# Performance work log

Hardware: AMD Instinct MI355X
Metric: run time of the kernel (lower is better)

## Reference

```python
import jax, jax.numpy as jnp
import numpy as np


def smooth_l1(x, y):
    d = jnp.abs(x - y)
    return jnp.where(d < 1.0, 0.5 * d * d, d - 0.5)


def setup_inputs() -> dict:
    key = jax.random.key(0)
    k1, k2, k3 = jax.random.split(key, 3)
    B, T, N, D = 4, 28, 1024, 3
    X_v = jax.random.normal(k1, (B, T, N, D), dtype=jnp.float32)
    target_X_v = jax.random.normal(k2, (B, T, N, D), dtype=jnp.float32)
    weights = jax.random.uniform(k3, (B, T), dtype=jnp.float32)
    return {"X_v": X_v, "target_X_v": target_X_v, "weights": weights}


def reference(X_v, target_X_v, weights):
    B = X_v.shape[0]
    # Pairwise squared distances [B,T,N,N] via ||p||^2 + ||t||^2 - 2 p.t
    pn = jnp.sum(X_v * X_v, axis=-1)                 # [B,T,N]
    tn = jnp.sum(target_X_v * target_X_v, axis=-1)   # [B,T,N]
    dist = (pn[..., :, None] + tn[..., None, :]
            - 2.0 * jnp.einsum('btnd,btmd->btnm', X_v, target_X_v))
    minv = jnp.argmin(dist, axis=-1)                 # [B,T,N] int
    # gather nearest target point for each pred point
    tagp = jnp.take_along_axis(target_X_v, minv[..., None], axis=2)  # [B,T,N,3]
    # per-(b,t) mean smooth-L1 over N points x 3 coords
    loss_bt = jnp.mean(smooth_l1(X_v, tagp), axis=(-2, -1))          # [B,T]
    loss = jnp.sum(loss_bt * weights) / B

    prec = jnp.mean(X_v, axis=2)        # [B,T,3]
    tarc = jnp.mean(target_X_v, axis=2) # [B,T,3]
    lossc = jnp.sum(smooth_l1(prec, tarc)) / (B * 3)
    return (loss, lossc)
```

## Files before the change

kernel.cpp:

```cpp
#include <hip/hip_runtime.h>

constexpr int Bc = 4;
constexpr int Tc = 28;
constexpr int Nc = 1024;
constexpr int Dc = 3;
constexpr int BT = Bc * Tc;
constexpr float OFFS = 512.0f;

constexpr int WS_PARTIAL = 0;
constexpr int WS_PSUM    = 224;
constexpr int WS_TSUM    = 224 + 224*3;

__device__ __forceinline__ float sl1(float d) {
    d = fabsf(d);
    return d < 1.0f ? 0.5f * d * d : d - 0.5f;
}

__global__ __launch_bounds__(256) void chamfer_kernel(
    const float* __restrict__ X, const float* __restrict__ Tg,
    const float* __restrict__ W, float* __restrict__ ws)
{
    __shared__ float4 sT4[Nc];
    __shared__ float sred[4][8];

    const int bt  = blockIdx.x >> 1;
    const int ph  = blockIdx.x & 1;
    const int tid = threadIdx.x;

    const float* xb = X + (size_t)bt * (Nc * Dc);
    const int n0 = ph * 512 + tid;
    const int n1 = n0 + 256;
    const float pAx = xb[n0 * 3 + 0], pAy = xb[n0 * 3 + 1], pAz = xb[n0 * 3 + 2];
    const float pBx = xb[n1 * 3 + 0], pBy = xb[n1 * 3 + 1], pBz = xb[n1 * 3 + 2];

    const float4* tg4 = (const float4*)(Tg + (size_t)bt * (Nc * Dc));
    const float4 r0 = tg4[3 * tid + 0];
    const float4 r1 = tg4[3 * tid + 1];
    const float4 r2 = tg4[3 * tid + 2];
    sT4[4 * tid + 0] = make_float4(r0.x, r0.y, r0.z, fmaf(r0.x, r0.x, fmaf(r0.y, r0.y, fmaf(r0.z, r0.z, OFFS))));
    sT4[4 * tid + 1] = make_float4(r0.w, r1.x, r1.y, fmaf(r0.w, r0.w, fmaf(r1.x, r1.x, fmaf(r1.y, r1.y, OFFS))));
    sT4[4 * tid + 2] = make_float4(r1.z, r1.w, r2.x, fmaf(r1.z, r1.z, fmaf(r1.w, r1.w, fmaf(r2.x, r2.x, OFFS))));
    sT4[4 * tid + 3] = make_float4(r2.y, r2.z, r2.w, fmaf(r2.y, r2.y, fmaf(r2.z, r2.z, fmaf(r2.w, r2.w, OFFS))));
    const float tsx = r0.x + r0.w + r1.z + r2.y;
    const float tsy = r0.y + r1.x + r1.w + r2.z;
    const float tsz = r0.z + r1.y + r2.x + r2.w;
    __syncthreads();

    const float cA0 = -2.0f * pAx, cA1 = -2.0f * pAy, cA2 = -2.0f * pAz;
    const float cB0 = -2.0f * pBx, cB1 = -2.0f * pBy, cB2 = -2.0f * pBz;

    float bestA = 3.4e38f, bestB = 3.4e38f;
    int iA = 0, iB = 0;

    constexpr int PF = 8;
    float4 bufA[PF], bufB[PF];

    #pragma unroll
    for (int j = 0; j < PF; ++j) bufA[j] = sT4[j];

    for (int m0 = 0; m0 < Nc; m0 += 2 * PF) {
        #pragma unroll
        for (int j = 0; j < PF; ++j) bufB[j] = sT4[m0 + PF + j];
        #pragma unroll
        for (int j = 0; j < PF; ++j) {
            const float4 t = bufA[j];
            const int m = m0 + j;
            float vA = fmaf(cA0, t.x, fmaf(cA1, t.y, fmaf(cA2, t.z, t.w)));
            float vB = fmaf(cB0, t.x, fmaf(cB1, t.y, fmaf(cB2, t.z, t.w)));
            bool ca = vA < bestA; bestA = ca ? vA : bestA; iA = ca ? m : iA;
            bool cb = vB < bestB; bestB = cb ? vB : bestB; iB = cb ? m : iB;
        }
        #pragma unroll
        for (int j = 0; j < PF; ++j) bufA[j] = sT4[(m0 + 2 * PF + j) & (Nc - 1)];
        #pragma unroll
        for (int j = 0; j < PF; ++j) {
            const float4 t = bufB[j];
            const int m = m0 + PF + j;
            float vA = fmaf(cA0, t.x, fmaf(cA1, t.y, fmaf(cA2, t.z, t.w)));
            float vB = fmaf(cB0, t.x, fmaf(cB1, t.y, fmaf(cB2, t.z, t.w)));
            bool ca = vA < bestA; bestA = ca ? vA : bestA; iA = ca ? m : iA;
            bool cb = vB < bestB; bestB = cb ? vB : bestB; iB = cb ? m : iB;
        }
    }

    const float4 tA = sT4[iA];
    const float4 tB = sT4[iB];
    float s = sl1(pAx - tA.x) + sl1(pAy - tA.y) + sl1(pAz - tA.z)
            + sl1(pBx - tB.x) + sl1(pBy - tB.y) + sl1(pBz - tB.z);

    float vals[7] = { s, pAx + pBx, pAy + pBy, pAz + pBz, tsx, tsy, tsz };
    const int lane = tid & 63, wid = tid >> 6;
    #pragma unroll
    for (int k = 0; k < 7; ++k) {
        float v = vals[k];
        #pragma unroll
        for (int off = 32; off; off >>= 1) v += __shfl_down(v, off, 64);
        if (lane == 0) sred[wid][k] = v;
    }
    __syncthreads();
    if (tid == 0) {
        float tot[7];
        #pragma unroll
        for (int k = 0; k < 7; ++k)
            tot[k] = sred[0][k] + sred[1][k] + sred[2][k] + sred[3][k];
        ws[WS_PARTIAL + blockIdx.x] = tot[0] * W[bt];
        ws[WS_PSUM + blockIdx.x * 3 + 0] = tot[1];
        ws[WS_PSUM + blockIdx.x * 3 + 1] = tot[2];
        ws[WS_PSUM + blockIdx.x * 3 + 2] = tot[3];
        if (ph == 0) {
            ws[WS_TSUM + bt * 3 + 0] = tot[4];
            ws[WS_TSUM + bt * 3 + 1] = tot[5];
            ws[WS_TSUM + bt * 3 + 2] = tot[6];
        }
    }
}

__global__ __launch_bounds__(256) void finalize_kernel(
    const float* __restrict__ ws, float* __restrict__ out)
{
    __shared__ float sred[4][2];
    const int tid = threadIdx.x;

    float lp = (tid < 224) ? ws[WS_PARTIAL + tid] : 0.0f;

    float lc = 0.0f;
    if (tid < BT) {
        const float inv = 1.0f / Nc;
        #pragma unroll
        for (int c = 0; c < 3; ++c) {
            float pm = (ws[WS_PSUM + (2 * tid) * 3 + c] + ws[WS_PSUM + (2 * tid + 1) * 3 + c]) * inv;
            float tm = ws[WS_TSUM + tid * 3 + c] * inv;
            lc += sl1(pm - tm);
        }
    }

    const int lane = tid & 63, wid = tid >> 6;
    #pragma unroll
    for (int off = 32; off; off >>= 1) {
        lp += __shfl_down(lp, off, 64);
        lc += __shfl_down(lc, off, 64);
    }
    if (lane == 0) { sred[wid][0] = lp; sred[wid][1] = lc; }
    __syncthreads();
    if (tid == 0) {
        float tlp = sred[0][0] + sred[1][0] + sred[2][0] + sred[3][0];
        float tlc = sred[0][1] + sred[1][1] + sred[2][1] + sred[3][1];
        out[0] = tlp * (1.0f / (Nc * Dc)) * (1.0f / Bc);
        out[1] = tlc * (1.0f / (Bc * Dc));
    }
}

extern "C" void kernel_launch(void* const* d_in, const int* in_sizes, int n_in,
                              void* d_out, int out_size, void* d_ws, size_t ws_size,
                              hipStream_t stream) {
    const float* X  = (const float*)d_in[0];
    const float* Tg = (const float*)d_in[1];
    const float* W  = (const float*)d_in[2];
    float* out = (float*)d_out;
    float* ws  = (float*)d_ws;

    chamfer_kernel<<<BT * 2, 256, 0, stream>>>(X, Tg, W, ws);
    finalize_kernel<<<1, 256, 0, stream>>>(ws, out);
}
```

Before: 88.61 us.

## Pack targets in a prep kernel and read them via uniform global loads

Adds a prep kernel that packs the target points with their squared norms into a float4 workspace and computes the centroid sums. The main kernel drops its shared-memory staging and barrier and reads the packed targets straight from global memory, where every lane loads the same address (a broadcast that should become scalar or cached loads). This aims to remove LDS traffic from the inner loop, but it adds one kernel launch and a workspace round trip. The OFFS bias added to the norms is also removed.

```diff
diff --git a/kernel.cpp b/kernel.cpp
--- a/kernel.cpp
+++ b/kernel.cpp
@@ -5,24 +5,71 @@
 constexpr int Nc = 1024;
 constexpr int Dc = 3;
 constexpr int BT = Bc * Tc;
-constexpr float OFFS = 512.0f;
 
-constexpr int WS_PARTIAL = 0;
-constexpr int WS_PSUM    = 224;
-constexpr int WS_TSUM    = 224 + 224*3;
+constexpr size_t WS_PACKED_F4 = 0;
+constexpr size_t WS_PARTIAL   = (size_t)BT * Nc * 4;
+constexpr size_t WS_PSUM      = WS_PARTIAL + 224;
+constexpr size_t WS_TSUM      = WS_PSUM + BT * 3;
 
 __device__ __forceinline__ float sl1(float d) {
     d = fabsf(d);
     return d < 1.0f ? 0.5f * d * d : d - 0.5f;
 }
 
+__global__ __launch_bounds__(256) void prep_kernel(
+    const float* __restrict__ X, const float* __restrict__ Tg,
+    float4* __restrict__ packed, float* __restrict__ sums)
+{
+    __shared__ float sred[4][8];
+    const int bt  = blockIdx.x;
+    const int tid = threadIdx.x;
+
+    const float4* tg4 = (const float4*)(Tg + (size_t)bt * (Nc * Dc));
+    const float4 r0 = tg4[3 * tid + 0];
+    const float4 r1 = tg4[3 * tid + 1];
+    const float4 r2 = tg4[3 * tid + 2];
+    float4* pk = packed + (size_t)bt * Nc;
+    pk[4 * tid + 0] = make_float4(r0.x, r0.y, r0.z, fmaf(r0.x, r0.x, fmaf(r0.y, r0.y, r0.z * r0.z)));
+    pk[4 * tid + 1] = make_float4(r0.w, r1.x, r1.y, fmaf(r0.w, r0.w, fmaf(r1.x, r1.x, r1.y * r1.y)));
+    pk[4 * tid + 2] = make_float4(r1.z, r1.w, r2.x, fmaf(r1.z, r1.z, fmaf(r1.w, r1.w, r2.x * r2.x)));
+    pk[4 * tid + 3] = make_float4(r2.y, r2.z, r2.w, fmaf(r2.y, r2.y, fmaf(r2.z, r2.z, r2.w * r2.w)));
+
+    const float4* x4 = (const float4*)(X + (size_t)bt * (Nc * Dc));
+    const float4 a0 = x4[3 * tid + 0];
+    const float4 a1 = x4[3 * tid + 1];
+    const float4 a2 = x4[3 * tid + 2];
+
+    float vals[6] = {
+        a0.x + a0.w + a1.z + a2.y,
+        a0.y + a1.x + a1.w + a2.z,
+        a0.z + a1.y + a2.x + a2.w,
+        r0.x + r0.w + r1.z + r2.y,
+        r0.y + r1.x + r1.w + r2.z,
+        r0.z + r1.y + r2.x + r2.w
+    };
+    const int lane = tid & 63, wid = tid >> 6;
+    #pragma unroll
+    for (int k = 0; k < 6; ++k) {
+        float v = vals[k];
+        #pragma unroll
+        for (int off = 32; off; off >>= 1) v += __shfl_down(v, off, 64);
+        if (lane == 0) sred[wid][k] = v;
+    }
+    __syncthreads();
+    if (tid == 0) {
+        #pragma unroll
+        for (int k = 0; k < 3; ++k) {
+            sums[WS_PSUM - WS_PARTIAL + bt * 3 + k] = sred[0][k] + sred[1][k] + sred[2][k] + sred[3][k];
+            sums[WS_TSUM - WS_PARTIAL + bt * 3 + k] = sred[0][k + 3] + sred[1][k + 3] + sred[2][k + 3] + sred[3][k + 3];
+        }
+    }
+}
+
 __global__ __launch_bounds__(256) void chamfer_kernel(
-    const float* __restrict__ X, const float* __restrict__ Tg,
-    const float* __restrict__ W, float* __restrict__ ws)
+    const float* __restrict__ X, const float4* __restrict__ packed,
+    const float* __restrict__ W, float* __restrict__ partial)
 {
-    __shared__ float4 sT4[Nc];
-    __shared__ float sred[4][8];
-
+    __shared__ float sred[4];
     const int bt  = blockIdx.x >> 1;
     const int ph  = blockIdx.x & 1;
     const int tid = threadIdx.x;
@@ -33,21 +80,10 @@
     const float pAx = xb[n0 * 3 + 0], pAy = xb[n0 * 3 + 1], pAz = xb[n0 * 3 + 2];
     const float pBx = xb[n1 * 3 + 0], pBy = xb[n1 * 3 + 1], pBz = xb[n1 * 3 + 2];
 
-    const float4* tg4 = (const float4*)(Tg + (size_t)bt * (Nc * Dc));
-    const float4 r0 = tg4[3 * tid + 0];
-    const float4 r1 = tg4[3 * tid + 1];
-    const float4 r2 = tg4[3 * tid + 2];
-    sT4[4 * tid + 0] = make_float4(r0.x, r0.y, r0.z, fmaf(r0.x, r0.x, fmaf(r0.y, r0.y, fmaf(r0.z, r0.z, OFFS))));
-    sT4[4 * tid + 1] = make_float4(r0.w, r1.x, r1.y, fmaf(r0.w, r0.w, fmaf(r1.x, r1.x, fmaf(r1.y, r1.y, OFFS))));
-    sT4[4 * tid + 2] = make_float4(r1.z, r1.w, r2.x, fmaf(r1.z, r1.z, fmaf(r1.w, r1.w, fmaf(r2.x, r2.x, OFFS))));
-    sT4[4 * tid + 3] = make_float4(r2.y, r2.z, r2.w, fmaf(r2.y, r2.y, fmaf(r2.z, r2.z, fmaf(r2.w, r2.w, OFFS))));
-    const float tsx = r0.x + r0.w + r1.z + r2.y;
-    const float tsy = r0.y + r1.x + r1.w + r2.z;
-    const float tsz = r0.z + r1.y + r2.x + r2.w;
-    __syncthreads();
-
     const float cA0 = -2.0f * pAx, cA1 = -2.0f * pAy, cA2 = -2.0f * pAz;
     const float cB0 = -2.0f * pBx, cB1 = -2.0f * pBy, cB2 = -2.0f * pBz;
+
+    const float4* __restrict__ pk = packed + (size_t)bt * Nc;
 
     float bestA = 3.4e38f, bestB = 3.4e38f;
     int iA = 0, iB = 0;
@@ -56,11 +92,11 @@
     float4 bufA[PF], bufB[PF];
 
     #pragma unroll
-    for (int j = 0; j < PF; ++j) bufA[j] = sT4[j];
+    for (int j = 0; j < PF; ++j) bufA[j] = pk[j];
 
     for (int m0 = 0; m0 < Nc; m0 += 2 * PF) {
         #pragma unroll
-        for (int j = 0; j < PF; ++j) bufB[j] = sT4[m0 + PF + j];
+        for (int j = 0; j < PF; ++j) bufB[j] = pk[m0 + PF + j];
         #pragma unroll
         for (int j = 0; j < PF; ++j) {
             const float4 t = bufA[j];
@@ -71,7 +107,7 @@
             bool cb = vB < bestB; bestB = cb ? vB : bestB; iB = cb ? m : iB;
         }
         #pragma unroll
-        for (int j = 0; j < PF; ++j) bufA[j] = sT4[(m0 + 2 * PF + j) & (Nc - 1)];
+        for (int j = 0; j < PF; ++j) bufA[j] = pk[(m0 + 2 * PF + j) & (Nc - 1)];
         #pragma unroll
         for (int j = 0; j < PF; ++j) {
             const float4 t = bufB[j];
@@ -83,53 +119,35 @@
         }
     }
 
-    const float4 tA = sT4[iA];
-    const float4 tB = sT4[iB];
+    const float4 tA = pk[iA];
+    const float4 tB = pk[iB];
     float s = sl1(pAx - tA.x) + sl1(pAy - tA.y) + sl1(pAz - tA.z)
             + sl1(pBx - tB.x) + sl1(pBy - tB.y) + sl1(pBz - tB.z);
 
-    float vals[7] = { s, pAx + pBx, pAy + pBy, pAz + pBz, tsx, tsy, tsz };
     const int lane = tid & 63, wid = tid >> 6;
     #pragma unroll
-    for (int k = 0; k < 7; ++k) {
-        float v = vals[k];
-        #pragma unroll
-        for (int off = 32; off; off >>= 1) v += __shfl_down(v, off, 64);
-        if (lane == 0) sred[wid][k] = v;
-    }
+    for (int off = 32; off; off >>= 1) s += __shfl_down(s, off, 64);
+    if (lane == 0) sred[wid] = s;
     __syncthreads();
-    if (tid == 0) {
-        float tot[7];
-        #pragma unroll
-        for (int k = 0; k < 7; ++k)
-            tot[k] = sred[0][k] + sred[1][k] + sred[2][k] + sred[3][k];
-        ws[WS_PARTIAL + blockIdx.x] = tot[0] * W[bt];
-        ws[WS_PSUM + blockIdx.x * 3 + 0] = tot[1];
-        ws[WS_PSUM + blockIdx.x * 3 + 1] = tot[2];
-        ws[WS_PSUM + blockIdx.x * 3 + 2] = tot[3];
-        if (ph == 0) {
-            ws[WS_TSUM + bt * 3 + 0] = tot[4];
-            ws[WS_TSUM + bt * 3 + 1] = tot[5];
-            ws[WS_TSUM + bt * 3 + 2] = tot[6];
-        }
-    }
+    if (tid == 0)
+        partial[blockIdx.x] = (sred[0] + sred[1] + sred[2] + sred[3]) * W[bt];
 }
 
 __global__ __launch_bounds__(256) void finalize_kernel(
-    const float* __restrict__ ws, float* __restrict__ out)
+    const float* __restrict__ sums, float* __restrict__ out)
 {
     __shared__ float sred[4][2];
     const int tid = threadIdx.x;
 
-    float lp = (tid < 224) ? ws[WS_PARTIAL + tid] : 0.0f;
+    float lp = (tid < 224) ? sums[tid] : 0.0f;
 
     float lc = 0.0f;
     if (tid < BT) {
         const float inv = 1.0f / Nc;
         #pragma unroll
         for (int c = 0; c < 3; ++c) {
-            float pm = (ws[WS_PSUM + (2 * tid) * 3 + c] + ws[WS_PSUM + (2 * tid + 1) * 3 + c]) * inv;
-            float tm = ws[WS_TSUM + tid * 3 + c] * inv;
+            float pm = sums[WS_PSUM - WS_PARTIAL + tid * 3 + c] * inv;
+            float tm = sums[WS_TSUM - WS_PARTIAL + tid * 3 + c] * inv;
             lc += sl1(pm - tm);
         }
     }
@@ -157,8 +175,11 @@
     const float* Tg = (const float*)d_in[1];
     const float* W  = (const float*)d_in[2];
     float* out = (float*)d_out;
-    float* ws  = (float*)d_ws;
 
-    chamfer_kernel<<<BT * 2, 256, 0, stream>>>(X, Tg, W, ws);
-    finalize_kernel<<<1, 256, 0, stream>>>(ws, out);
+    float4* packed = (float4*)d_ws;
+    float*  sums   = (float*)d_ws + WS_PARTIAL;
+
+    prep_kernel<<<BT, 256, 0, stream>>>(X, Tg, packed, sums);
+    chamfer_kernel<<<BT * 2, 256, 0, stream>>>(X, packed, W, sums );
+    finalize_kernel<<<1, 256, 0, stream>>>(sums, out);
 }
```

New measurement: 105.5 us. +19.1%, slower.

## Split target search into quarters across blocks with separate gather kernel

Applied to the files above, without the earlier changes.

The nearest-neighbour search is split so each block scans only a quarter of the target points, which raises the grid from 224 to 896 blocks to fill more compute units. Per-quarter best values and indices go to global workspace, and a new gather kernel picks the global argmin, gathers the target point and does the smooth-L1 reduction. This adds a kernel launch and global traffic for the partial results, and it drops the constant offset previously added to the squared norm. The __syncthreads sits inside a block-uniform branch (th==0), so it is safe.

```diff
diff --git a/kernel.cpp b/kernel.cpp
--- a/kernel.cpp
+++ b/kernel.cpp
@@ -5,26 +5,30 @@
 constexpr int Nc = 1024;
 constexpr int Dc = 3;
 constexpr int BT = Bc * Tc;
-constexpr float OFFS = 512.0f;
-
-constexpr int WS_PARTIAL = 0;
-constexpr int WS_PSUM    = 224;
-constexpr int WS_TSUM    = 224 + 224*3;
+constexpr int QT = 256;
+
+constexpr size_t WS_BESTV   = 0;
+constexpr size_t WS_BESTI   = (size_t)BT * Nc * 4;
+constexpr size_t WS_PARTIAL = WS_BESTI + (size_t)BT * Nc * 4;
+constexpr size_t WS_PSUM    = WS_PARTIAL + 224;
+constexpr size_t WS_TSUM    = WS_PSUM + BT * 2 * 3;
 
 __device__ __forceinline__ float sl1(float d) {
     d = fabsf(d);
     return d < 1.0f ? 0.5f * d * d : d - 0.5f;
 }
 
-__global__ __launch_bounds__(256) void chamfer_kernel(
+__global__ __launch_bounds__(256) void chamfer_quarter_kernel(
     const float* __restrict__ X, const float* __restrict__ Tg,
-    const float* __restrict__ W, float* __restrict__ ws)
+    float* __restrict__ bestv, int* __restrict__ besti,
+    float* __restrict__ psum, float* __restrict__ tsum)
 {
-    __shared__ float4 sT4[Nc];
-    __shared__ float sred[4][8];
-
-    const int bt  = blockIdx.x >> 1;
-    const int ph  = blockIdx.x & 1;
+    __shared__ float4 sT4[QT];
+    __shared__ float sred[4][3];
+
+    const int bt  = blockIdx.x >> 3;
+    const int ph  = (blockIdx.x >> 2) & 1;
+    const int th  = blockIdx.x & 3;
     const int tid = threadIdx.x;
 
     const float* xb = X + (size_t)bt * (Nc * Dc);
@@ -33,17 +37,32 @@
     const float pAx = xb[n0 * 3 + 0], pAy = xb[n0 * 3 + 1], pAz = xb[n0 * 3 + 2];
     const float pBx = xb[n1 * 3 + 0], pBy = xb[n1 * 3 + 1], pBz = xb[n1 * 3 + 2];
 
-    const float4* tg4 = (const float4*)(Tg + (size_t)bt * (Nc * Dc));
-    const float4 r0 = tg4[3 * tid + 0];
-    const float4 r1 = tg4[3 * tid + 1];
-    const float4 r2 = tg4[3 * tid + 2];
-    sT4[4 * tid + 0] = make_float4(r0.x, r0.y, r0.z, fmaf(r0.x, r0.x, fmaf(r0.y, r0.y, fmaf(r0.z, r0.z, OFFS))));
-    sT4[4 * tid + 1] = make_float4(r0.w, r1.x, r1.y, fmaf(r0.w, r0.w, fmaf(r1.x, r1.x, fmaf(r1.y, r1.y, OFFS))));
-    sT4[4 * tid + 2] = make_float4(r1.z, r1.w, r2.x, fmaf(r1.z, r1.z, fmaf(r1.w, r1.w, fmaf(r2.x, r2.x, OFFS))));
-    sT4[4 * tid + 3] = make_float4(r2.y, r2.z, r2.w, fmaf(r2.y, r2.y, fmaf(r2.z, r2.z, fmaf(r2.w, r2.w, OFFS))));
-    const float tsx = r0.x + r0.w + r1.z + r2.y;
-    const float tsy = r0.y + r1.x + r1.w + r2.z;
-    const float tsz = r0.z + r1.y + r2.x + r2.w;
+    if (tid < 64) {
+        const float4* tg4 = (const float4*)(Tg + (size_t)bt * (Nc * Dc) + th * (QT * 3));
+        const float4 r0 = tg4[3 * tid + 0];
+        const float4 r1 = tg4[3 * tid + 1];
+        const float4 r2 = tg4[3 * tid + 2];
+        sT4[4 * tid + 0] = make_float4(r0.x, r0.y, r0.z, fmaf(r0.x, r0.x, fmaf(r0.y, r0.y, r0.z * r0.z)));
+        sT4[4 * tid + 1] = make_float4(r0.w, r1.x, r1.y, fmaf(r0.w, r0.w, fmaf(r1.x, r1.x, r1.y * r1.y)));
+        sT4[4 * tid + 2] = make_float4(r1.z, r1.w, r2.x, fmaf(r1.z, r1.z, fmaf(r1.w, r1.w, r2.x * r2.x)));
+        sT4[4 * tid + 3] = make_float4(r2.y, r2.z, r2.w, fmaf(r2.y, r2.y, fmaf(r2.z, r2.z, r2.w * r2.w)));
+        if (ph == 0) {
+            float tx = r0.x + r0.w + r1.z + r2.y;
+            float ty = r0.y + r1.x + r1.w + r2.z;
+            float tz = r0.z + r1.y + r2.x + r2.w;
+            #pragma unroll
+            for (int off = 32; off; off >>= 1) {
+                tx += __shfl_down(tx, off, 64);
+                ty += __shfl_down(ty, off, 64);
+                tz += __shfl_down(tz, off, 64);
+            }
+            if (tid == 0) {
+                tsum[(bt * 4 + th) * 3 + 0] = tx;
+                tsum[(bt * 4 + th) * 3 + 1] = ty;
+                tsum[(bt * 4 + th) * 3 + 2] = tz;
+            }
+        }
+    }
     __syncthreads();
 
     const float cA0 = -2.0f * pAx, cA1 = -2.0f * pAy, cA2 = -2.0f * pAz;
@@ -54,11 +73,10 @@
 
     constexpr int PF = 8;
     float4 bufA[PF], bufB[PF];
-
     #pragma unroll
     for (int j = 0; j < PF; ++j) bufA[j] = sT4[j];
 
-    for (int m0 = 0; m0 < Nc; m0 += 2 * PF) {
+    for (int m0 = 0; m0 < QT; m0 += 2 * PF) {
         #pragma unroll
         for (int j = 0; j < PF; ++j) bufB[j] = sT4[m0 + PF + j];
         #pragma unroll
@@ -71,7 +89,7 @@
             bool cb = vB < bestB; bestB = cb ? vB : bestB; iB = cb ? m : iB;
         }
         #pragma unroll
-        for (int j = 0; j < PF; ++j) bufA[j] = sT4[(m0 + 2 * PF + j) & (Nc - 1)];
+        for (int j = 0; j < PF; ++j) bufA[j] = sT4[(m0 + 2 * PF + j) & (QT - 1)];
         #pragma unroll
         for (int j = 0; j < PF; ++j) {
             const float4 t = bufB[j];
@@ -83,36 +101,68 @@
         }
     }
 
-    const float4 tA = sT4[iA];
-    const float4 tB = sT4[iB];
-    float s = sl1(pAx - tA.x) + sl1(pAy - tA.y) + sl1(pAz - tA.z)
-            + sl1(pBx - tB.x) + sl1(pBy - tB.y) + sl1(pBz - tB.z);
-
-    float vals[7] = { s, pAx + pBx, pAy + pBy, pAz + pBz, tsx, tsy, tsz };
+    const size_t base = (size_t)bt * Nc;
+    bestv[(base + n0) * 4 + th] = bestA;
+    bestv[(base + n1) * 4 + th] = bestB;
+    besti[(base + n0) * 4 + th] = th * QT + iA;
+    besti[(base + n1) * 4 + th] = th * QT + iB;
+
+    if (th == 0) {
+        float sx = pAx + pBx, sy = pAy + pBy, sz = pAz + pBz;
+        const int lane = tid & 63, wid = tid >> 6;
+        #pragma unroll
+        for (int off = 32; off; off >>= 1) {
+            sx += __shfl_down(sx, off, 64);
+            sy += __shfl_down(sy, off, 64);
+            sz += __shfl_down(sz, off, 64);
+        }
+        if (lane == 0) { sred[wid][0] = sx; sred[wid][1] = sy; sred[wid][2] = sz; }
+        __syncthreads();
+        if (tid == 0) {
+            #pragma unroll
+            for (int k = 0; k < 3; ++k)
+                psum[(bt * 2 + ph) * 3 + k] = sred[0][k] + sred[1][k] + sred[2][k] + sred[3][k];
+        }
+    }
+}
+
+__global__ __launch_bounds__(256) void gather_kernel(
+    const float* __restrict__ X, const float* __restrict__ Tg,
+    const float* __restrict__ W,
+    const float4* __restrict__ bestv4, const int4* __restrict__ besti4,
+    float* __restrict__ partial)
+{
+    __shared__ float sred[4];
+    const int bt  = blockIdx.x >> 1;
+    const int ph  = blockIdx.x & 1;
+    const int tid = threadIdx.x;
+
+    const float* xb = X  + (size_t)bt * (Nc * Dc);
+    const float* tb = Tg + (size_t)bt * (Nc * Dc);
+    const size_t base = (size_t)bt * Nc;
+
+    float s = 0.0f;
+    #pragma unroll
+    for (int p = 0; p < 2; ++p) {
+        const int n = ph * 512 + p * 256 + tid;
+        const float4 bv = bestv4[base + n];
+        const int4   bi = besti4[base + n];
+        float best = bv.x; int idx = bi.x;
+        if (bv.y < best) { best = bv.y; idx = bi.y; }
+        if (bv.z < best) { best = bv.z; idx = bi.z; }
+        if (bv.w < best) { best = bv.w; idx = bi.w; }
+        const float px = xb[n * 3 + 0], py = xb[n * 3 + 1], pz = xb[n * 3 + 2];
+        const float tx = tb[idx * 3 + 0], ty = tb[idx * 3 + 1], tz = tb[idx * 3 + 2];
+        s += sl1(px - tx) + sl1(py - ty) + sl1(pz - tz);
+    }
+
     const int lane = tid & 63, wid = tid >> 6;
     #pragma unroll
-    for (int k = 0; k < 7; ++k) {
-        float v = vals[k];
-        #pragma unroll
-        for (int off = 32; off; off >>= 1) v += __shfl_down(v, off, 64);
-        if (lane == 0) sred[wid][k] = v;
-    }
+    for (int off = 32; off; off >>= 1) s += __shfl_down(s, off, 64);
+    if (lane == 0) sred[wid] = s;
     __syncthreads();
-    if (tid == 0) {
-        float tot[7];
-        #pragma unroll
-        for (int k = 0; k < 7; ++k)
-            tot[k] = sred[0][k] + sred[1][k] + sred[2][k] + sred[3][k];
-        ws[WS_PARTIAL + blockIdx.x] = tot[0] * W[bt];
-        ws[WS_PSUM + blockIdx.x * 3 + 0] = tot[1];
-        ws[WS_PSUM + blockIdx.x * 3 + 1] = tot[2];
-        ws[WS_PSUM + blockIdx.x * 3 + 2] = tot[3];
-        if (ph == 0) {
-            ws[WS_TSUM + bt * 3 + 0] = tot[4];
-            ws[WS_TSUM + bt * 3 + 1] = tot[5];
-            ws[WS_TSUM + bt * 3 + 2] = tot[6];
-        }
-    }
+    if (tid == 0)
+        partial[blockIdx.x] = (sred[0] + sred[1] + sred[2] + sred[3]) * W[bt];
 }
 
 __global__ __launch_bounds__(256) void finalize_kernel(
@@ -129,7 +179,8 @@
         #pragma unroll
         for (int c = 0; c < 3; ++c) {
             float pm = (ws[WS_PSUM + (2 * tid) * 3 + c] + ws[WS_PSUM + (2 * tid + 1) * 3 + c]) * inv;
-            float tm = ws[WS_TSUM + tid * 3 + c] * inv;
+            float tm = (ws[WS_TSUM + (4 * tid) * 3 + c] + ws[WS_TSUM + (4 * tid + 1) * 3 + c]
+                      + ws[WS_TSUM + (4 * tid + 2) * 3 + c] + ws[WS_TSUM + (4 * tid + 3) * 3 + c]) * inv;
             lc += sl1(pm - tm);
         }
     }
@@ -159,6 +210,13 @@
     float* out = (float*)d_out;
     float* ws  = (float*)d_ws;
 
-    chamfer_kernel<<<BT * 2, 256, 0, stream>>>(X, Tg, W, ws);
+    float* bestv = ws + WS_BESTV;
+    int*   besti = (int*)(ws + WS_BESTI);
+    float* psum  = ws + WS_PSUM;
+    float* tsum  = ws + WS_TSUM;
+
+    chamfer_quarter_kernel<<<BT * 8, 256, 0, stream>>>(X, Tg, bestv, besti, psum, tsum);
+    gather_kernel<<<BT * 2, 256, 0, stream>>>(X, Tg, W,
+        (const float4*)(ws + WS_BESTV), (const int4*)(ws + WS_BESTI), ws + WS_PARTIAL);
     finalize_kernel<<<1, 256, 0, stream>>>(ws, out);
 }
```

Result: no change. 88.72 us (+0.1%).
